# Kernel optimization log

Measured on AMD Instinct MI355X. Metric: run time of the kernel, lower is better.

## Reference

```python
import jax, jax.numpy as jnp
import numpy as np
import math

B, N, D = 16, 1024, 1024

def setup_inputs() -> dict:
    key = jax.random.key(0)
    k1, k2, k3, k4 = jax.random.split(key, 4)
    x = jax.random.normal(k1, (B, N, D), dtype=jnp.float32)
    # Keras 'random_normal' initializer defaults to stddev=0.05
    w_keys = jax.random.normal(k2, (N, N), dtype=jnp.float32) * 0.05
    w_queries = jax.random.normal(k3, (N, N), dtype=jnp.float32) * 0.05
    w_values = jax.random.normal(k4, (N, N), dtype=jnp.float32) * 0.05
    return {"x": x, "w_keys": w_keys, "w_queries": w_queries, "w_values": w_values}

def reference(x, w_keys, w_queries, w_values):
    # x: (B, N, D); weights: (N, N); fact = sqrt(N) per build(input_shape[1])
    fact = math.sqrt(x.shape[1])
    ip = jnp.swapaxes(x, 1, 2)              # (B, D, N)
    vk = ip @ w_keys                         # (B, D, N)
    vq = ip @ w_queries                      # (B, D, N)
    vv = ip @ w_values                       # (B, D, N)
    kq = jnp.einsum('bdn,ben->bde', vk, vq) / fact   # (B, D, D)
    sm = jax.nn.softmax(kq, axis=-1)         # softmax over last axis
    # tf: sm @ transpose(pm(vv)) == sm @ vv  since pm then transpose_b cancel
    out = jnp.einsum('bde,ben->bdn', sm, vv) # (B, D, N)
    return jnp.swapaxes(out, 1, 2)           # (B, N, D)
```

## Files before the change

kernel.cpp:

```cpp
#include <hip/hip_runtime.h>
#include <stdint.h>


typedef __bf16 bf16x8_t __attribute__((ext_vector_type(8)));
typedef float  f32x4_t  __attribute__((ext_vector_type(4)));

typedef __attribute__((address_space(3))) uint32_t as3_u32;
typedef __attribute__((address_space(1))) uint32_t as1_u32;

__device__ __forceinline__ void async_copy16(const void* g, const void* l) {
  __builtin_amdgcn_global_load_lds((const as1_u32*)(uintptr_t)g,
                                   (as3_u32*)(uint32_t)(uintptr_t)l,
                                   16, 0, 0);
}

__device__ __forceinline__ uint16_t f2bf(float f) {
  uint32_t x = __float_as_uint(f);
  return (uint16_t)((x + 0x7fffu + ((x >> 16) & 1u)) >> 16);
}
__device__ __forceinline__ float bf2f(uint16_t b) {
  return __uint_as_float(((uint32_t)b) << 16);
}

template <int EPI>
__device__ __forceinline__ void gemm_body(
    const uint16_t* __restrict__ A, const uint16_t* __restrict__ B,
    void* __restrict__ Cv, size_t sA, size_t sB, size_t sC,
    float alpha, float* __restrict__ Sp, int lid, char* smem)
{
  char* As = smem;
  char* Bs = smem + 32768;

  const int xcd  = lid & 7;
  const int slot = lid >> 3;
  const int z    = (xcd << 1) | (slot >> 5);
  const int t32  = slot & 31;
  const int bm0  = (t32 >> 3) << 8;
  const int bn0  = (t32 & 7) << 7;

  A += (size_t)z * sA + ((size_t)bm0 << 10);
  B += (size_t)z * sB + ((size_t)bn0 << 10);

  const int t    = threadIdx.x;
  const int lane = t & 63;
  const int w    = t >> 6;
  const int q    = lane >> 4;
  const int r16  = lane & 15;
  const int wm   = (w >> 1) << 6;
  const int wn   = (w & 1) << 6;

  const int g0  = t >> 3;
  const int cp  = t & 7;
  const int ce  = (cp ^ (g0 & 7)) << 3;
  const int so  = (g0 << 7) + (cp << 4);
  const uint16_t* Ag = A + ((size_t)g0 << 10) + ce;
  const uint16_t* Bg = B + ((size_t)g0 << 10) + ce;

  f32x4_t acc[4][4];
#pragma unroll
  for (int i = 0; i < 4; i++)
#pragma unroll
    for (int j = 0; j < 4; j++) acc[i][j] = (f32x4_t){0.f, 0.f, 0.f, 0.f};

  for (int k0 = 0; k0 < 1024; k0 += 64) {
#pragma unroll
    for (int s = 0; s < 4; ++s)
      async_copy16(Ag + (((size_t)s << 6) << 10) + k0, As + so + (s << 13));
#pragma unroll
    for (int s = 0; s < 2; ++s)
      async_copy16(Bg + (((size_t)s << 6) << 10) + k0, Bs + so + (s << 13));
    __syncthreads();

#pragma unroll
    for (int kk = 0; kk < 2; ++kk) {
      bf16x8_t af[4], bfr[4];
#pragma unroll
      for (int mi = 0; mi < 4; ++mi) {
        const int m = wm + (mi << 4) + r16;
        const int c = (kk << 2) + q;
        af[mi] = *(const bf16x8_t*)(As + (m << 7) + ((c ^ (m & 7)) << 4));
      }
#pragma unroll
      for (int ni = 0; ni < 4; ++ni) {
        const int n = wn + (ni << 4) + r16;
        const int c = (kk << 2) + q;
        bfr[ni] = *(const bf16x8_t*)(Bs + (n << 7) + ((c ^ (n & 7)) << 4));
      }
      __builtin_amdgcn_s_setprio(1);
#pragma unroll
      for (int mi = 0; mi < 4; ++mi)
#pragma unroll
        for (int ni = 0; ni < 4; ++ni)
          acc[mi][ni] = __builtin_amdgcn_mfma_f32_16x16x32_bf16(
              af[mi], bfr[ni], acc[mi][ni], 0, 0, 0);
      __builtin_amdgcn_s_setprio(0);
    }
    __syncthreads();
  }

  if constexpr (EPI == 3) {
    float inv[4];
#pragma unroll
    for (int ni = 0; ni < 4; ++ni) {
      const int c = bn0 + wn + (ni << 4) + r16;
      float S = 0.f;
#pragma unroll
      for (int p = 0; p < 16; ++p)
        S += Sp[((size_t)p << 14) + ((size_t)z << 10) + c];
      inv[ni] = 1.0f / S;
    }
    float* C = (float*)Cv + (size_t)z * sC;
#pragma unroll
    for (int mi = 0; mi < 4; ++mi)
#pragma unroll
      for (int ni = 0; ni < 4; ++ni)
#pragma unroll
        for (int r = 0; r < 4; ++r) {
          const int row = bm0 + wm + (mi << 4) + (q << 2) + r;
          const int col = bn0 + wn + (ni << 4) + r16;
          C[((size_t)row << 10) + col] = acc[mi][ni][r] * alpha * inv[ni];
        }
  } else {
    float* reg = (float*)smem + (size_t)w * 1056;
    uint16_t* C = (uint16_t*)Cv + (size_t)z * sC;
    float* SpW = Sp + ((size_t)(((bn0 >> 7) << 1) + (w & 1)) << 14)
                    + ((size_t)z << 10);
#pragma unroll
    for (int mi = 0; mi < 4; ++mi) {
      if constexpr (EPI == 2) {
        float ev[4][4];
#pragma unroll
        for (int ni = 0; ni < 4; ++ni)
#pragma unroll
          for (int r = 0; r < 4; ++r) {
            ev[ni][r] = __expf(acc[mi][ni][r] * alpha);
            reg[((q << 2) + r) * 66 + (ni << 4) + r16] = ev[ni][r];
          }
#pragma unroll
        for (int r = 0; r < 4; ++r) {
          float s = ev[0][r] + ev[1][r] + ev[2][r] + ev[3][r];
          s += __shfl_xor(s, 1, 16);
          s += __shfl_xor(s, 2, 16);
          s += __shfl_xor(s, 4, 16);
          s += __shfl_xor(s, 8, 16);
          if (r16 == 0)
            SpW[bm0 + wm + (mi << 4) + (q << 2) + r] = s;
        }
      } else {
#pragma unroll
        for (int ni = 0; ni < 4; ++ni)
#pragma unroll
          for (int r = 0; r < 4; ++r)
            reg[((q << 2) + r) * 66 + (ni << 4) + r16] = acc[mi][ni][r] * alpha;
      }
#pragma unroll
      for (int it = 0; it < 8; ++it) {
        const int rr = (it << 1) + (lane >> 5);
        const int cc = (lane & 31) << 1;
        const float2 v = *(const float2*)(reg + rr * 66 + cc);
        const uint32_t p = (uint32_t)f2bf(v.x) | ((uint32_t)f2bf(v.y) << 16);
        const int row = bm0 + wm + (mi << 4) + rr;
        const int col = bn0 + wn + cc;
        *(uint32_t*)(C + ((size_t)row << 10) + col) = p;
      }
    }
  }
}

template <int EPI>
__global__ __launch_bounds__(512, 4)
void gemm_bt256x128(const uint16_t* __restrict__ A,
                    const uint16_t* __restrict__ B,
                    void* __restrict__ Cv, size_t sA, size_t sB, size_t sC,
                    float alpha, float* __restrict__ Sp)
{
  __shared__ __align__(16) char smem[49152];
  gemm_body<EPI>(A, B, Cv, sA, sB, sC, alpha, Sp, blockIdx.x, smem);
}

__global__ __launch_bounds__(512, 4)
void gemm_pair(const uint16_t* __restrict__ A0, const uint16_t* __restrict__ B0,
               void* __restrict__ C0, size_t sA0, size_t sB0, size_t sC0,
               const uint16_t* __restrict__ A1, const uint16_t* __restrict__ B1,
               void* __restrict__ C1, size_t sA1, size_t sB1, size_t sC1)
{
  __shared__ __align__(16) char smem[49152];
  const int lid = blockIdx.x;
  if (lid < 512)
    gemm_body<0>(A0, B0, C0, sA0, sB0, sC0, 1.0f, nullptr, lid, smem);
  else
    gemm_body<0>(A1, B1, C1, sA1, sB1, sC1, 1.0f, nullptr, lid - 512, smem);
}

__global__ __launch_bounds__(256)
void prep_all(const float* __restrict__ x, uint16_t* __restrict__ xT,
              const float* __restrict__ wq, const float* __restrict__ wk,
              const float* __restrict__ wv, float* __restrict__ W2p,
              uint16_t* __restrict__ Wtv)
{
  __shared__ __align__(16) char smem[32768];
  const int bx = blockIdx.x;
  const int t  = threadIdx.x;

  if (bx < 256) {
    char* As = smem;
    char* Bs = smem + 16384;
    const int slice = bx >> 6;
    const int tile4 = bx & 63;
    const int bm0   = (tile4 >> 3) << 7;
    const int bn0   = (tile4 & 7) << 7;
    const int koff  = slice << 8;
    const int lane = t & 63;
    const int w4 = t >> 6;
    const int q = lane >> 4;
    const int r16 = lane & 15;
    const int wm = (w4 >> 1) << 6;
    const int wn = (w4 & 1) << 6;
    const int g0 = t >> 1;
    const int kh = (t & 1) << 5;
    const float* srcA = wq + (size_t)(bm0 + g0) * 1024 + kh;
    const float* srcB = wk + (size_t)(bn0 + g0) * 1024 + kh;

    f32x4_t acc[4][4];
#pragma unroll
    for (int i = 0; i < 4; i++)
#pragma unroll
      for (int j = 0; j < 4; j++) acc[i][j] = (f32x4_t){0.f, 0.f, 0.f, 0.f};

    for (int k0 = koff; k0 < koff + 256; k0 += 64) {
#pragma unroll
      for (int j = 0; j < 4; ++j) {
        const int c  = ((t & 1) << 2) + j;
        const int cp = c ^ (g0 & 7);
        const float4 a0 = *(const float4*)(srcA + k0 + (j << 3));
        const float4 a1 = *(const float4*)(srcA + k0 + (j << 3) + 4);
        const float4 b0 = *(const float4*)(srcB + k0 + (j << 3));
        const float4 b1 = *(const float4*)(srcB + k0 + (j << 3) + 4);
        uint4 pa, pb;
        pa.x = (uint32_t)f2bf(a0.x) | ((uint32_t)f2bf(a0.y) << 16);
        pa.y = (uint32_t)f2bf(a0.z) | ((uint32_t)f2bf(a0.w) << 16);
        pa.z = (uint32_t)f2bf(a1.x) | ((uint32_t)f2bf(a1.y) << 16);
        pa.w = (uint32_t)f2bf(a1.z) | ((uint32_t)f2bf(a1.w) << 16);
        pb.x = (uint32_t)f2bf(b0.x) | ((uint32_t)f2bf(b0.y) << 16);
        pb.y = (uint32_t)f2bf(b0.z) | ((uint32_t)f2bf(b0.w) << 16);
        pb.z = (uint32_t)f2bf(b1.x) | ((uint32_t)f2bf(b1.y) << 16);
        pb.w = (uint32_t)f2bf(b1.z) | ((uint32_t)f2bf(b1.w) << 16);
        *(uint4*)(As + (g0 << 7) + (cp << 4)) = pa;
        *(uint4*)(Bs + (g0 << 7) + (cp << 4)) = pb;
      }
      __syncthreads();
#pragma unroll
      for (int kk = 0; kk < 2; kk++) {
        bf16x8_t af[4], bfr[4];
#pragma unroll
        for (int mi = 0; mi < 4; mi++) {
          const int m = wm + (mi << 4) + r16;
          const int c = (kk << 2) + q;
          af[mi] = *(const bf16x8_t*)(As + (m << 7) + ((c ^ (m & 7)) << 4));
        }
#pragma unroll
        for (int ni = 0; ni < 4; ni++) {
          const int n = wn + (ni << 4) + r16;
          const int c = (kk << 2) + q;
          bfr[ni] = *(const bf16x8_t*)(Bs + (n << 7) + ((c ^ (n & 7)) << 4));
        }
#pragma unroll
        for (int mi = 0; mi < 4; mi++)
#pragma unroll
          for (int ni = 0; ni < 4; ni++)
            acc[mi][ni] = __builtin_amdgcn_mfma_f32_16x16x32_bf16(
                af[mi], bfr[ni], acc[mi][ni], 0, 0, 0);
      }
      __syncthreads();
    }
    float* C = W2p + (size_t)slice * (1024u * 1024u);
#pragma unroll
    for (int mi = 0; mi < 4; mi++)
#pragma unroll
      for (int ni = 0; ni < 4; ni++)
#pragma unroll
        for (int r = 0; r < 4; r++) {
          const int row = bm0 + wm + (mi << 4) + (q << 2) + r;
          const int col = bn0 + wn + (ni << 4) + r16;
          C[((size_t)row << 10) + col] = acc[mi][ni][r];
        }
    return;
  }

  if (bx < 4352) {
    float (*tile)[65] = (float(*)[65])smem;
    const int bxx = bx - 256;
    const int z  = bxx >> 8;
    const int r0 = ((bxx >> 4) & 15) << 6;
    const int c0 = (bxx & 15) << 6;
    const float* src = x + ((size_t)z << 20);
    uint16_t* dst = xT + ((size_t)z << 20);
    const int row  = t >> 4;
    const int col4 = (t & 15) << 2;
#pragma unroll
    for (int i = 0; i < 4; ++i) {
      const float4 v = *(const float4*)(
          src + (size_t)(r0 + row + (i << 4)) * 1024 + c0 + col4);
      float* tp = &tile[row + (i << 4)][col4];
      tp[0] = v.x; tp[1] = v.y; tp[2] = v.z; tp[3] = v.w;
    }
    __syncthreads();
#pragma unroll
    for (int p = 0; p < 2; ++p) {
      const int idx = (p << 8) + t;
      const int c  = idx >> 3;
      const int s8 = (idx & 7) << 3;
      uint32_t u0 = (uint32_t)f2bf(tile[s8 + 0][c]) |
                    ((uint32_t)f2bf(tile[s8 + 1][c]) << 16);
      uint32_t u1 = (uint32_t)f2bf(tile[s8 + 2][c]) |
                    ((uint32_t)f2bf(tile[s8 + 3][c]) << 16);
      uint32_t u2 = (uint32_t)f2bf(tile[s8 + 4][c]) |
                    ((uint32_t)f2bf(tile[s8 + 5][c]) << 16);
      uint32_t u3 = (uint32_t)f2bf(tile[s8 + 6][c]) |
                    ((uint32_t)f2bf(tile[s8 + 7][c]) << 16);
      uint4 pk; pk.x = u0; pk.y = u1; pk.z = u2; pk.w = u3;
      *(uint4*)(dst + (size_t)(c0 + c) * 1024 + r0 + s8) = pk;
    }
    return;
  }

  {
    float (*tile)[33] = (float(*)[33])smem;
    const int bxw = bx - 4352;
    const int r0 = (bxw >> 5) << 5;
    const int c0 = (bxw & 31) << 5;
    const int tx = t & 31, ty = t >> 5;
#pragma unroll
    for (int i = 0; i < 32; i += 8)
      tile[ty + i][tx] = wv[(size_t)(r0 + ty + i) * 1024 + (c0 + tx)];
    __syncthreads();
#pragma unroll
    for (int i = 0; i < 32; i += 8)
      Wtv[(size_t)(c0 + ty + i) * 1024 + (r0 + tx)] = f2bf(tile[tx][ty + i]);
  }
}

__global__ __launch_bounds__(256)
void reduce_w2t(const float* __restrict__ P, uint16_t* __restrict__ W)
{
  const size_t i4 = (((size_t)blockIdx.x << 8) + threadIdx.x) << 2;
  const float4 a = *(const float4*)(P + i4);
  const float4 b = *(const float4*)(P + (1u << 20) + i4);
  const float4 c = *(const float4*)(P + (2u << 20) + i4);
  const float4 d = *(const float4*)(P + (3u << 20) + i4);
  ushort4 r;
  r.x = f2bf(a.x + b.x + c.x + d.x);
  r.y = f2bf(a.y + b.y + c.y + d.y);
  r.z = f2bf(a.z + b.z + c.z + d.z);
  r.w = f2bf(a.w + b.w + c.w + d.w);
  *(ushort4*)(W + i4) = r;
}

extern "C" void kernel_launch(void* const* d_in, const int* in_sizes, int n_in,
                              void* d_out, int out_size, void* d_ws, size_t ws_size,
                              hipStream_t stream)
{
  const float* x  = (const float*)d_in[0];
  const float* wk = (const float*)d_in[1];
  const float* wq = (const float*)d_in[2];
  const float* wv = (const float*)d_in[3];
  float* out = (float*)d_out;

  constexpr int N = 1024;
  constexpr size_t DN = (size_t)N * N;

  char* ws = (char*)d_ws;
  uint16_t* xT   = (uint16_t*)(ws);
  uint16_t* Wtv  = (uint16_t*)(ws + (36ull << 20));
  uint16_t* W2Tc = (uint16_t*)(ws + (38ull << 20));
  float*    W2p  = (float*)   (ws + (40ull << 20));
  uint16_t* tmp  = (uint16_t*)(ws + (56ull << 20));
  uint16_t* vvT  = (uint16_t*)(ws + (88ull << 20));
  uint16_t* P    = (uint16_t*)(ws + (120ull << 20));
  float*    Spart= (float*)   (ws + (152ull << 20));

  prep_all<<<5376, 256, 0, stream>>>(x, xT, wq, wk, wv, W2p, Wtv);
  reduce_w2t<<<1024, 256, 0, stream>>>(W2p, W2Tc);
  gemm_pair<<<1024, 512, 0, stream>>>(xT, W2Tc, tmp, DN, 0, DN,
                                      Wtv, xT, vvT, 0, DN, DN);
  gemm_bt256x128<2><<<512, 512, 0, stream>>>(tmp, xT, P, DN, DN, DN, 0.03125f, Spart);
  gemm_bt256x128<3><<<512, 512, 0, stream>>>(vvT, P, out, DN, DN, DN, 1.0f, Spart);
}
```

Baseline: 276.2 us.

## Fuse score and output GEMMs into one launch with per-stripe atomic flags

Result: slower. 294.6 us (+6.7%).

```diff
diff --git a/kernel.cpp b/kernel.cpp
--- a/kernel.cpp
+++ b/kernel.cpp
@@ -167,17 +167,6 @@
   }
 }
 
-template <int EPI>
-__global__ __launch_bounds__(512, 4)
-void gemm_bt256x128(const uint16_t* __restrict__ A,
-                    const uint16_t* __restrict__ B,
-                    void* __restrict__ Cv, size_t sA, size_t sB, size_t sC,
-                    float alpha, float* __restrict__ Sp)
-{
-  __shared__ __align__(16) char smem[49152];
-  gemm_body<EPI>(A, B, Cv, sA, sB, sC, alpha, Sp, blockIdx.x, smem);
-}
-
 __global__ __launch_bounds__(512, 4)
 void gemm_pair(const uint16_t* __restrict__ A0, const uint16_t* __restrict__ B0,
                void* __restrict__ C0, size_t sA0, size_t sB0, size_t sC0,
@@ -192,11 +181,48 @@
     gemm_body<0>(A1, B1, C1, sA1, sB1, sC1, 1.0f, nullptr, lid - 512, smem);
 }
 
+__global__ __launch_bounds__(512, 4)
+void gemm_po(const uint16_t* __restrict__ tmp, const uint16_t* __restrict__ xT,
+             uint16_t* __restrict__ P, const uint16_t* __restrict__ vvT,
+             float* __restrict__ out, float* __restrict__ Sp,
+             int* __restrict__ flags)
+{
+  __shared__ __align__(16) char smem[49152];
+  const int bx = blockIdx.x;
+  constexpr size_t DN = 1024ull * 1024ull;
+
+  if (bx < 512) {
+    gemm_body<2>(tmp, xT, P, DN, DN, DN, 0.03125f, Sp, bx, smem);
+    __syncthreads();
+    if (threadIdx.x == 0) {
+      const int xcd  = bx & 7;
+      const int slot = bx >> 3;
+      const int z    = (xcd << 1) | (slot >> 5);
+      const int strp = (slot & 31) >> 3;
+      __hip_atomic_fetch_add(&flags[(z << 2) + strp], 1,
+                             __ATOMIC_RELEASE, __HIP_MEMORY_SCOPE_AGENT);
+    }
+  } else {
+    const int lid  = bx - 512;
+    const int xcd  = lid & 7;
+    const int slot = lid >> 3;
+    const int z    = (xcd << 1) | (slot >> 5);
+    const int strp = ((slot & 31) & 7) >> 1;
+    if (threadIdx.x == 0) {
+      while (__hip_atomic_load(&flags[(z << 2) + strp],
+                               __ATOMIC_ACQUIRE, __HIP_MEMORY_SCOPE_AGENT) < 8)
+        __builtin_amdgcn_s_sleep(8);
+    }
+    __syncthreads();
+    gemm_body<3>(vvT, P, out, DN, DN, DN, 1.0f, Sp, lid, smem);
+  }
+}
+
 __global__ __launch_bounds__(256)
 void prep_all(const float* __restrict__ x, uint16_t* __restrict__ xT,
               const float* __restrict__ wq, const float* __restrict__ wk,
               const float* __restrict__ wv, float* __restrict__ W2p,
-              uint16_t* __restrict__ Wtv)
+              uint16_t* __restrict__ Wtv, int* __restrict__ flags)
 {
   __shared__ __align__(16) char smem[32768];
   const int bx = blockIdx.x;
@@ -337,6 +363,7 @@
 #pragma unroll
     for (int i = 0; i < 32; i += 8)
       Wtv[(size_t)(c0 + ty + i) * 1024 + (r0 + tx)] = f2bf(tile[tx][ty + i]);
+    if (bx == 5375 && t < 64) flags[t] = 0;
   }
 }
 
@@ -378,11 +405,11 @@
   uint16_t* vvT  = (uint16_t*)(ws + (88ull << 20));
   uint16_t* P    = (uint16_t*)(ws + (120ull << 20));
   float*    Spart= (float*)   (ws + (152ull << 20));
-
-  prep_all<<<5376, 256, 0, stream>>>(x, xT, wq, wk, wv, W2p, Wtv);
+  int*      flags= (int*)     (ws + (153ull << 20));
+
+  prep_all<<<5376, 256, 0, stream>>>(x, xT, wq, wk, wv, W2p, Wtv, flags);
   reduce_w2t<<<1024, 256, 0, stream>>>(W2p, W2Tc);
   gemm_pair<<<1024, 512, 0, stream>>>(xT, W2Tc, tmp, DN, 0, DN,
                                       Wtv, xT, vvT, 0, DN, DN);
-  gemm_bt256x128<2><<<512, 512, 0, stream>>>(tmp, xT, P, DN, DN, DN, 0.03125f, Spart);
-  gemm_bt256x128<3><<<512, 512, 0, stream>>>(vvT, P, out, DN, DN, DN, 1.0f, Spart);
-}
+  gemm_po<<<1024, 512, 0, stream>>>(tmp, xT, P, vvT, out, Spart, flags);
+}
```

## Use 256x256 tiles with 64-wide K steps for the paired projection GEMMs

Applied to the files above, without the earlier changes.

Measured after the change: 850.8 us. 3.08x slower.

```diff
diff --git a/kernel.cpp b/kernel.cpp
--- a/kernel.cpp
+++ b/kernel.cpp
@@ -127,31 +127,23 @@
                     + ((size_t)z << 10);
 #pragma unroll
     for (int mi = 0; mi < 4; ++mi) {
-      if constexpr (EPI == 2) {
-        float ev[4][4];
-#pragma unroll
-        for (int ni = 0; ni < 4; ++ni)
-#pragma unroll
-          for (int r = 0; r < 4; ++r) {
-            ev[ni][r] = __expf(acc[mi][ni][r] * alpha);
-            reg[((q << 2) + r) * 66 + (ni << 4) + r16] = ev[ni][r];
-          }
+      float ev[4][4];
+#pragma unroll
+      for (int ni = 0; ni < 4; ++ni)
 #pragma unroll
         for (int r = 0; r < 4; ++r) {
-          float s = ev[0][r] + ev[1][r] + ev[2][r] + ev[3][r];
-          s += __shfl_xor(s, 1, 16);
-          s += __shfl_xor(s, 2, 16);
-          s += __shfl_xor(s, 4, 16);
-          s += __shfl_xor(s, 8, 16);
-          if (r16 == 0)
-            SpW[bm0 + wm + (mi << 4) + (q << 2) + r] = s;
+          ev[ni][r] = __expf(acc[mi][ni][r] * alpha);
+          reg[((q << 2) + r) * 66 + (ni << 4) + r16] = ev[ni][r];
         }
-      } else {
-#pragma unroll
-        for (int ni = 0; ni < 4; ++ni)
-#pragma unroll
-          for (int r = 0; r < 4; ++r)
-            reg[((q << 2) + r) * 66 + (ni << 4) + r16] = acc[mi][ni][r] * alpha;
+#pragma unroll
+      for (int r = 0; r < 4; ++r) {
+        float s = ev[0][r] + ev[1][r] + ev[2][r] + ev[3][r];
+        s += __shfl_xor(s, 1, 16);
+        s += __shfl_xor(s, 2, 16);
+        s += __shfl_xor(s, 4, 16);
+        s += __shfl_xor(s, 8, 16);
+        if (r16 == 0)
+          SpW[bm0 + wm + (mi << 4) + (q << 2) + r] = s;
       }
 #pragma unroll
       for (int it = 0; it < 8; ++it) {
@@ -178,18 +170,115 @@
   gemm_body<EPI>(A, B, Cv, sA, sB, sC, alpha, Sp, blockIdx.x, smem);
 }
 
+__device__ __forceinline__ void gemm_body256(
+    const uint16_t* __restrict__ A, const uint16_t* __restrict__ B,
+    uint16_t* __restrict__ Cg, size_t sA, size_t sB, size_t sC,
+    int lid, char* smem)
+{
+  char* As = smem;
+  char* Bs = smem + 32768;
+
+  const int xcd  = lid & 7;
+  const int slot = lid >> 3;
+  const int z    = (xcd << 1) | (slot >> 4);
+  const int t16  = slot & 15;
+  const int bm0  = (t16 >> 2) << 8;
+  const int bn0  = (t16 & 3) << 8;
+
+  A += (size_t)z * sA + ((size_t)bm0 << 10);
+  B += (size_t)z * sB + ((size_t)bn0 << 10);
+
+  const int t    = threadIdx.x;
+  const int lane = t & 63;
+  const int w    = t >> 6;
+  const int q    = lane >> 4;
+  const int r16  = lane & 15;
+  const int wm   = (w >> 2) << 7;
+  const int wn   = (w & 3) << 6;
+
+  const int g0  = t >> 3;
+  const int cp  = t & 7;
+  const int ce  = (cp ^ (g0 & 7)) << 3;
+  const int so  = (g0 << 7) + (cp << 4);
+  const uint16_t* Ag = A + ((size_t)g0 << 10) + ce;
+  const uint16_t* Bg = B + ((size_t)g0 << 10) + ce;
+
+  f32x4_t acc[8][4];
+#pragma unroll
+  for (int i = 0; i < 8; i++)
+#pragma unroll
+    for (int j = 0; j < 4; j++) acc[i][j] = (f32x4_t){0.f, 0.f, 0.f, 0.f};
+
+  for (int k0 = 0; k0 < 1024; k0 += 64) {
+#pragma unroll
+    for (int s = 0; s < 4; ++s)
+      async_copy16(Ag + (((size_t)s << 6) << 10) + k0, As + so + (s << 13));
+#pragma unroll
+    for (int s = 0; s < 4; ++s)
+      async_copy16(Bg + (((size_t)s << 6) << 10) + k0, Bs + so + (s << 13));
+    __syncthreads();
+
+#pragma unroll
+    for (int kk = 0; kk < 2; ++kk) {
+      bf16x8_t af[8], bfr[4];
+#pragma unroll
+      for (int mi = 0; mi < 8; ++mi) {
+        const int m = wm + (mi << 4) + r16;
+        const int c = (kk << 2) + q;
+        af[mi] = *(const bf16x8_t*)(As + (m << 7) + ((c ^ (m & 7)) << 4));
+      }
+#pragma unroll
+      for (int ni = 0; ni < 4; ++ni) {
+        const int n = wn + (ni << 4) + r16;
+        const int c = (kk << 2) + q;
+        bfr[ni] = *(const bf16x8_t*)(Bs + (n << 7) + ((c ^ (n & 7)) << 4));
+      }
+      __builtin_amdgcn_s_setprio(1);
+#pragma unroll
+      for (int mi = 0; mi < 8; ++mi)
+#pragma unroll
+        for (int ni = 0; ni < 4; ++ni)
+          acc[mi][ni] = __builtin_amdgcn_mfma_f32_16x16x32_bf16(
+              af[mi], bfr[ni], acc[mi][ni], 0, 0, 0);
+      __builtin_amdgcn_s_setprio(0);
+    }
+    __syncthreads();
+  }
+
+  float* reg = (float*)smem + (size_t)w * 1056;
+  uint16_t* C = Cg + (size_t)z * sC;
+#pragma unroll
+  for (int mi = 0; mi < 8; ++mi) {
+#pragma unroll
+    for (int ni = 0; ni < 4; ++ni)
+#pragma unroll
+      for (int r = 0; r < 4; ++r)
+        reg[((q << 2) + r) * 66 + (ni << 4) + r16] = acc[mi][ni][r];
+#pragma unroll
+    for (int it = 0; it < 8; ++it) {
+      const int rr = (it << 1) + (lane >> 5);
+      const int cc = (lane & 31) << 1;
+      const float2 v = *(const float2*)(reg + rr * 66 + cc);
+      const uint32_t p = (uint32_t)f2bf(v.x) | ((uint32_t)f2bf(v.y) << 16);
+      const int row = bm0 + wm + (mi << 4) + rr;
+      const int col = bn0 + wn + cc;
+      *(uint32_t*)(C + ((size_t)row << 10) + col) = p;
+    }
+  }
+}
+
 __global__ __launch_bounds__(512, 4)
 void gemm_pair(const uint16_t* __restrict__ A0, const uint16_t* __restrict__ B0,
-               void* __restrict__ C0, size_t sA0, size_t sB0, size_t sC0,
+               uint16_t* __restrict__ C0, size_t sA0, size_t sB0, size_t sC0,
                const uint16_t* __restrict__ A1, const uint16_t* __restrict__ B1,
-               void* __restrict__ C1, size_t sA1, size_t sB1, size_t sC1)
-{
-  __shared__ __align__(16) char smem[49152];
+               uint16_t* __restrict__ C1, size_t sA1, size_t sB1, size_t sC1)
+{
+  __shared__ __align__(16) char smem[65536];
   const int lid = blockIdx.x;
-  if (lid < 512)
-    gemm_body<0>(A0, B0, C0, sA0, sB0, sC0, 1.0f, nullptr, lid, smem);
+  if (lid < 256)
+    gemm_body256(A0, B0, C0, sA0, sB0, sC0, lid, smem);
   else
-    gemm_body<0>(A1, B1, C1, sA1, sB1, sC1, 1.0f, nullptr, lid - 512, smem);
+    gemm_body256(A1, B1, C1, sA1, sB1, sC1, lid - 256, smem);
 }
 
 __global__ __launch_bounds__(256)
@@ -381,8 +470,8 @@
 
   prep_all<<<5376, 256, 0, stream>>>(x, xT, wq, wk, wv, W2p, Wtv);
   reduce_w2t<<<1024, 256, 0, stream>>>(W2p, W2Tc);
-  gemm_pair<<<1024, 512, 0, stream>>>(xT, W2Tc, tmp, DN, 0, DN,
-                                      Wtv, xT, vvT, 0, DN, DN);
+  gemm_pair<<<512, 512, 0, stream>>>(xT, W2Tc, tmp, DN, 0, DN,
+                                     Wtv, xT, vvT, 0, DN, DN);
   gemm_bt256x128<2><<<512, 512, 0, stream>>>(tmp, xT, P, DN, DN, DN, 0.03125f, Spart);
   gemm_bt256x128<3><<<512, 512, 0, stream>>>(vvT, P, out, DN, DN, DN, 1.0f, Spart);
 }
```
